# Kernel tuning notes

Hardware: AMD Instinct MI355X
Metric: run time of the kernel (lower is better)

## Reference

```python
import jax, jax.numpy as jnp
import numpy as np

NUM_USERS = 100000
NUM_ITEMS = 50000
NUM_FEATS = 512
DIM = 32
E_SOC = 3200000
E_UI = 3200000
N_PAIRS = 1000000


def setup_inputs() -> dict:
    key = jax.random.key(0)
    ks = jax.random.split(key, 14)
    return {
        "user_features": jax.random.normal(ks[0], (NUM_USERS, NUM_FEATS), jnp.float32),
        "item_features": jax.random.normal(ks[1], (NUM_ITEMS, NUM_FEATS), jnp.float32),
        "user_embedding": 0.01 * jax.random.normal(ks[2], (NUM_USERS, DIM), jnp.float32),
        "item_embedding": 0.01 * jax.random.normal(ks[3], (NUM_ITEMS, DIM), jnp.float32),
        "wr_w": jax.random.normal(ks[4], (NUM_FEATS, DIM), jnp.float32) / np.sqrt(NUM_FEATS),
        "wr_b": jax.random.normal(ks[5], (DIM,), jnp.float32) * 0.01,
        "social_rows": jax.random.randint(ks[6], (E_SOC,), 0, NUM_USERS, jnp.int32),
        "social_cols": jax.random.randint(ks[7], (E_SOC,), 0, NUM_USERS, jnp.int32),
        "social_vals": jax.random.uniform(ks[8], (E_SOC,), jnp.float32),
        "ui_rows": jax.random.randint(ks[9], (E_UI,), 0, NUM_USERS, jnp.int32),
        "ui_cols": jax.random.randint(ks[10], (E_UI,), 0, NUM_ITEMS, jnp.int32),
        "ui_vals": jax.random.uniform(ks[11], (E_UI,), jnp.float32),
        "user_indices": jax.random.randint(ks[12], (N_PAIRS,), 0, NUM_USERS, jnp.int32),
        "item_indices": jax.random.randint(ks[13], (N_PAIRS,), 0, NUM_ITEMS, jnp.int32),
    }


def _normalize(x):
    # torch .mean()/.std() over ALL elements, std unbiased (ddof=1)
    return (x - x.mean()) / jnp.std(x, ddof=1)


def _spmm(rows, cols, vals, x, n_out):
    # COO sparse @ dense: out[r] += v * x[c]
    return jax.ops.segment_sum(vals[:, None] * x[cols], rows, num_segments=n_out)


def reference(user_features, item_features, user_embedding, item_embedding,
              wr_w, wr_b, social_rows, social_cols, social_vals,
              ui_rows, ui_cols, ui_vals, user_indices, item_indices):
    n_users = user_embedding.shape[0]
    # feature normalization (done in __init__ in the torch module)
    uf = _normalize(user_features)
    itf = _normalize(item_features)

    user_reduce = _normalize(jax.nn.sigmoid(uf @ wr_w + wr_b))
    user_fusion = user_reduce + user_embedding
    item_reduce = _normalize(jax.nn.sigmoid(itf @ wr_w + wr_b))
    item_fusion = item_embedding + item_reduce

    item_consumed = _spmm(ui_rows, ui_cols, ui_vals, item_fusion, n_users)
    h1 = _spmm(social_rows, social_cols, social_vals, user_fusion, n_users)
    h2 = _spmm(social_rows, social_cols, social_vals, h1, n_users)
    last_user_embedding = item_consumed + h2

    predict_vector = jnp.sum(last_user_embedding[user_indices] * item_fusion[item_indices], axis=1)
    predictions = jax.nn.sigmoid(predict_vector)
    return predict_vector, predictions
```

## Files before the change

### kernel.cpp

```cpp
#include <hip/hip_runtime.h>
#include <hip/hip_bf16.h>

#define NU 100000
#define NI 50000
#define NF 512
#define DIM 32
#define ES 3200000
#define EU 3200000
#define NP 1000000
#define CHUNK 1024
#define NCH 98

#define ABK 32
#define BRNG 3125
#define EHALF 1600000
#define ACAP 52000
#define ATILE 2048

typedef short bf16x8 __attribute__((ext_vector_type(8)));
typedef float f32x4 __attribute__((ext_vector_type(4)));

__device__ __forceinline__ float s2f(short s) {
    unsigned u = ((unsigned)(unsigned short)s) << 16;
    return __uint_as_float(u);
}
__device__ __forceinline__ short f2bf(float f) {
    unsigned u = __float_as_uint(f);
    return (short)((u + 0x7FFFu + ((u >> 16) & 1u)) >> 16);
}

__global__ void wsum_kernel(const float* __restrict__ W, float* __restrict__ wsum) {
    int c = threadIdx.x;
    if (c >= DIM) return;
    float s = 0.f;
    for (int k = 0; k < NF; ++k) s += W[k * DIM + c];
    wsum[c] = s;
}

__global__ __launch_bounds__(256) void gemm_stats_kernel(
    const float* __restrict__ X, const float* __restrict__ W,
    float* __restrict__ RAW, float* __restrict__ statSum, float* __restrict__ statSq,
    int M)
{
    __shared__ short bfrag[16384];
    for (int idx = threadIdx.x; idx < 16384; idx += 256) {
        int j = idx & 7;
        int lane = (idx >> 3) & 63;
        int t = (idx >> 9) & 1;
        int s = idx >> 10;
        int k = s * 32 + ((lane >> 4) << 3) + j;
        int n = t * 16 + (lane & 15);
        bfrag[idx] = f2bf(W[k * DIM + n]);
    }
    __syncthreads();

    const int wave = threadIdx.x >> 6;
    const int lane = threadIdx.x & 63;
    const int quad = lane >> 4;
    const int mrow = lane & 15;

    bf16x8 ones;
#pragma unroll
    for (int j = 0; j < 8; ++j) ones[j] = (short)0x3F80;

    float lsum = 0.f, lsq = 0.f;
    const int nstrips = M >> 4;
    for (int strip = blockIdx.x * 4 + wave; strip < nstrips; strip += gridDim.x * 4) {
        const float* arow = X + (size_t)(strip * 16 + mrow) * NF + quad * 8;
        f32x4 acc0 = {0.f, 0.f, 0.f, 0.f};
        f32x4 acc1 = {0.f, 0.f, 0.f, 0.f};
        f32x4 accR = {0.f, 0.f, 0.f, 0.f};
        f32x4 accG = {0.f, 0.f, 0.f, 0.f};
#pragma unroll
        for (int s = 0; s < 16; ++s) {
            float4 a0 = *(const float4*)(arow + s * 32);
            float4 a1 = *(const float4*)(arow + s * 32 + 4);
            bf16x8 a;
            a[0] = f2bf(a0.x); a[1] = f2bf(a0.y); a[2] = f2bf(a0.z); a[3] = f2bf(a0.w);
            a[4] = f2bf(a1.x); a[5] = f2bf(a1.y); a[6] = f2bf(a1.z); a[7] = f2bf(a1.w);
            bf16x8 b0 = *(const bf16x8*)(bfrag + (s * 2 + 0) * 512 + lane * 8);
            bf16x8 b1 = *(const bf16x8*)(bfrag + (s * 2 + 1) * 512 + lane * 8);
            acc0 = __builtin_amdgcn_mfma_f32_16x16x32_bf16(a, b0, acc0, 0, 0, 0);
            acc1 = __builtin_amdgcn_mfma_f32_16x16x32_bf16(a, b1, acc1, 0, 0, 0);
            accR = __builtin_amdgcn_mfma_f32_16x16x32_bf16(a, ones, accR, 0, 0, 0);
            accG = __builtin_amdgcn_mfma_f32_16x16x32_bf16(a, a, accG, 0, 0, 0);
        }
        float* outp = RAW + (size_t)strip * 16 * DIM;
#pragma unroll
        for (int i = 0; i < 4; ++i) {
            int r = quad * 4 + i;
            outp[r * DIM + mrow]      = acc0[i];
            outp[r * DIM + 16 + mrow] = acc1[i];
        }
        if (mrow == 0) lsum += (accR[0] + accR[1]) + (accR[2] + accR[3]);
        int dg = mrow - quad * 4;
        if (dg >= 0 && dg < 4) lsq += accG[dg];
    }
#pragma unroll
    for (int off = 32; off > 0; off >>= 1) {
        lsum += __shfl_down(lsum, off);
        lsq  += __shfl_down(lsq, off);
    }
    if (lane == 0) { atomicAdd(statSum, lsum); atomicAdd(statSq, lsq); }
}

__global__ __launch_bounds__(256) void signorm_kernel(
    float* __restrict__ buf, int n4, float nx,
    const float* __restrict__ statsIn, const float* __restrict__ wsum,
    const float* __restrict__ bias, float* __restrict__ statsOut)
{
    float mu  = statsIn[0] / nx;
    float var = (statsIn[1] - nx * mu * mu) / (nx - 1.f);
    float inv = 1.f / sqrtf(var);
    float ls = 0.f, lsq = 0.f;
    int stride = gridDim.x * blockDim.x;
    for (int i = blockIdx.x * blockDim.x + threadIdx.x; i < n4; i += stride) {
        float4 v = ((const float4*)buf)[i];
        int c0 = (i << 2) & 31;
        float4 r;
        r.x = 1.f / (1.f + expf(-((v.x - mu * wsum[c0 + 0]) * inv + bias[c0 + 0])));
        r.y = 1.f / (1.f + expf(-((v.y - mu * wsum[c0 + 1]) * inv + bias[c0 + 1])));
        r.z = 1.f / (1.f + expf(-((v.z - mu * wsum[c0 + 2]) * inv + bias[c0 + 2])));
        r.w = 1.f / (1.f + expf(-((v.w - mu * wsum[c0 + 3]) * inv + bias[c0 + 3])));
        ((float4*)buf)[i] = r;
        ls  += (r.x + r.y) + (r.z + r.w);
        lsq += (r.x * r.x + r.y * r.y) + (r.z * r.z + r.w * r.w);
    }
#pragma unroll
    for (int off = 32; off > 0; off >>= 1) {
        ls  += __shfl_down(ls, off);
        lsq += __shfl_down(lsq, off);
    }
    if ((threadIdx.x & 63) == 0) { atomicAdd(statsOut + 0, ls); atomicAdd(statsOut + 1, lsq); }
}

__global__ __launch_bounds__(256) void fusion_kernel(
    float* __restrict__ buf, const float* __restrict__ emb, int n4, float n,
    const float* __restrict__ statsIn)
{
    float mu  = statsIn[0] / n;
    float var = (statsIn[1] - n * mu * mu) / (n - 1.f);
    float inv = 1.f / sqrtf(var);
    int stride = gridDim.x * blockDim.x;
    for (int i = blockIdx.x * blockDim.x + threadIdx.x; i < n4; i += stride) {
        float4 v = ((const float4*)buf)[i];
        float4 e = ((const float4*)emb)[i];
        v.x = (v.x - mu) * inv + e.x;
        v.y = (v.y - mu) * inv + e.y;
        v.z = (v.z - mu) * inv + e.z;
        v.w = (v.w - mu) * inv + e.w;
        ((float4*)buf)[i] = v;
    }
}

__global__ void hist_kernel(const int* __restrict__ sr, const int* __restrict__ ur,
                            int* __restrict__ cntS, int* __restrict__ cntU)
{
    int i = blockIdx.x * 256 + threadIdx.x;
    if (i < ES) atomicAdd(cntS + sr[i], 1);
    else        atomicAdd(cntU + ur[i - ES], 1);
}

__global__ void chunksum_kernel(const int* __restrict__ cntS, const int* __restrict__ cntU,
                                int* __restrict__ csS, int* __restrict__ csU)
{
    int b = blockIdx.x;
    const int* cnt; int* cs; int c;
    if (b < NCH) { cnt = cntS; cs = csS; c = b; }
    else         { cnt = cntU; cs = csU; c = b - NCH; }
    int base = c * CHUNK;
    int v = 0;
    for (int t = threadIdx.x; t < CHUNK; t += 256) {
        int i = base + t;
        if (i < NU) v += cnt[i];
    }
#pragma unroll
    for (int off = 32; off > 0; off >>= 1) v += __shfl_down(v, off);
    __shared__ int sm[4];
    if ((threadIdx.x & 63) == 0) sm[threadIdx.x >> 6] = v;
    __syncthreads();
    if (threadIdx.x == 0) cs[c] = sm[0] + sm[1] + sm[2] + sm[3];
}

__global__ void scan_offsets_kernel(int* __restrict__ csS, int* __restrict__ csU,
                                    int* __restrict__ rpS, int* __restrict__ rpU)
{
    if (threadIdx.x == 0) {
        int run = 0;
        for (int c = 0; c < NCH; ++c) { int t = csS[c]; csS[c] = run; run += t; }
        rpS[NU] = run;
    }
    if (threadIdx.x == 1) {
        int run = 0;
        for (int c = 0; c < NCH; ++c) { int t = csU[c]; csU[c] = run; run += t; }
        rpU[NU] = run;
    }
}

__global__ __launch_bounds__(1024) void chunkscan_kernel(
    const int* __restrict__ cntS, const int* __restrict__ cntU,
    const int* __restrict__ csS, const int* __restrict__ csU,
    int* __restrict__ rpS, int* __restrict__ rpU)
{
    int b = blockIdx.x;
    const int* cnt; const int* cs; int* rp; int c;
    if (b < NCH) { cnt = cntS; cs = csS; rp = rpS; c = b; }
    else         { cnt = cntU; cs = csU; rp = rpU; c = b - NCH; }
    int i = c * CHUNK + threadIdx.x;
    int v = (i < NU) ? cnt[i] : 0;
    __shared__ int sm[CHUNK];
    sm[threadIdx.x] = v;
    __syncthreads();
    for (int off = 1; off < CHUNK; off <<= 1) {
        int t = (threadIdx.x >= off) ? sm[threadIdx.x - off] : 0;
        __syncthreads();
        sm[threadIdx.x] += t;
        __syncthreads();
    }
    if (i < NU) rp[i] = cs[c] + sm[threadIdx.x] - v;
}

__global__ __launch_bounds__(256) void bucketA_kernel(
    const int* __restrict__ rows, const int* __restrict__ cols, const float* __restrict__ vals,
    int estart, int eend,
    unsigned* __restrict__ gW, unsigned short* __restrict__ gR, int* __restrict__ gFill)
{
    __shared__ int cnt[ABK], base[ABK], gpos[ABK], rank[ABK];
    __shared__ unsigned bufW[ATILE];
    __shared__ unsigned short bufR[ATILE];
    __shared__ unsigned char bufB[ATILE];

    int e0 = estart + blockIdx.x * ATILE;
    int n = eend - e0; if (n > ATILE) n = ATILE;
    int tid = threadIdx.x;
    if (tid < ABK) { cnt[tid] = 0; rank[tid] = 0; }
    __syncthreads();

    unsigned w[8]; unsigned short rl[8]; unsigned char bb[8]; bool ok[8];
#pragma unroll
    for (int j = 0; j < 8; ++j) {
        int idx = tid + j * 256;
        ok[j] = idx < n;
        if (ok[j]) {
            int e = e0 + idx;
            unsigned r = (unsigned)rows[e];
            unsigned b = r / BRNG;
            bb[j] = (unsigned char)b;
            rl[j] = (unsigned short)(r - b * BRNG);
            w[j]  = (((unsigned)(unsigned short)f2bf(vals[e])) << 17) | (unsigned)cols[e];
            atomicAdd(&cnt[b], 1);
        }
    }
    __syncthreads();
    if (tid == 0) {
        int run = 0;
        for (int k = 0; k < ABK; ++k) { base[k] = run; run += cnt[k]; }
    }
    __syncthreads();
    if (tid < ABK) gpos[tid] = atomicAdd(gFill + tid, cnt[tid]);
#pragma unroll
    for (int j = 0; j < 8; ++j) {
        if (ok[j]) {
            int b = bb[j];
            int p = base[b] + atomicAdd(&rank[b], 1);
            bufW[p] = w[j]; bufR[p] = rl[j]; bufB[p] = (unsigned char)b;
        }
    }
    __syncthreads();
    for (int i = tid; i < n; i += 256) {
        int b = bufB[i];
        int dst = gpos[b] + (i - base[b]);
        if (dst < ACAP) {
            gW[b * ACAP + dst] = bufW[i];
            gR[b * ACAP + dst] = bufR[i];
        }
    }
}

__global__ __launch_bounds__(256) void bucketB_kernel(
    const unsigned* __restrict__ gW, const unsigned short* __restrict__ gR,
    const int* __restrict__ gFill, const int* __restrict__ rp,
    int* __restrict__ fill, unsigned* __restrict__ csr)
{
    int myx = blockIdx.x & 7;
    int gslot = blockIdx.x >> 3;
#pragma unroll
    for (int j = 0; j < 4; ++j) {
        int b = myx + 8 * j;
        int n = gFill[b]; if (n > ACAP) n = ACAP;
        int s0 = (int)((long long)n * gslot / 128);
        int s1 = (int)((long long)n * (gslot + 1) / 128);
        for (int i = s0 + threadIdx.x; i < s1; i += 256) {
            unsigned w = gW[b * ACAP + i];
            int r = b * BRNG + (int)gR[b * ACAP + i];
            int p = rp[r] + atomicAdd(fill + r, 1);
            csr[p] = w;
        }
    }
}

__global__ __launch_bounds__(256) void spmm_csr_kernel(
    const int* __restrict__ rp, const unsigned* __restrict__ csr,
    const float* __restrict__ X, float* __restrict__ out, int accum)
{
    int r = blockIdx.x * 8 + (threadIdx.x >> 5);
    int d = threadIdx.x & 31;
    int s = rp[r], e = rp[r + 1];
    float acc = accum ? out[(size_t)r * DIM + d] : 0.f;
    float acc2 = 0.f;
    int i = s;
    for (; i + 3 < e; i += 4) {
        unsigned a = csr[i];
        unsigned b = csr[i + 1];
        unsigned c = csr[i + 2];
        unsigned dd = csr[i + 3];
        acc  += s2f((short)(a >> 17))  * X[(size_t)(a & 0x1FFFF) * DIM + d];
        acc2 += s2f((short)(b >> 17))  * X[(size_t)(b & 0x1FFFF) * DIM + d];
        acc  += s2f((short)(c >> 17))  * X[(size_t)(c & 0x1FFFF) * DIM + d];
        acc2 += s2f((short)(dd >> 17)) * X[(size_t)(dd & 0x1FFFF) * DIM + d];
    }
    for (; i < e; ++i) {
        unsigned a = csr[i];
        acc += s2f((short)(a >> 17)) * X[(size_t)(a & 0x1FFFF) * DIM + d];
    }
    out[(size_t)r * DIM + d] = acc + acc2;
}

__global__ __launch_bounds__(256) void atomic_spmm_kernel(
    const int* __restrict__ rows, const int* __restrict__ cols,
    const float* __restrict__ vals, const float* __restrict__ X,
    float* __restrict__ out, int ne)
{
    int e = blockIdx.x * 8 + (threadIdx.x >> 5);
    if (e >= ne) return;
    int d = threadIdx.x & 31;
    int r = rows[e], c = cols[e];
    atomicAdd(out + (size_t)r * DIM + d, vals[e] * X[(size_t)c * DIM + d]);
}

__global__ __launch_bounds__(256) void pairs_kernel(
    const float* __restrict__ ACC, const float* __restrict__ IF,
    const int* __restrict__ ui, const int* __restrict__ ii,
    float* __restrict__ out)
{
    int p = blockIdx.x * 8 + (threadIdx.x >> 5);
    int d = threadIdx.x & 31;
    int u = ui[p], it = ii[p];
    float v = ACC[(size_t)u * DIM + d] * IF[(size_t)it * DIM + d];
    v += __shfl_xor(v, 1);
    v += __shfl_xor(v, 2);
    v += __shfl_xor(v, 4);
    v += __shfl_xor(v, 8);
    v += __shfl_xor(v, 16);
    if (d == 0) {
        out[p] = v;
        out[NP + p] = 1.f / (1.f + expf(-v));
    }
}

extern "C" void kernel_launch(void* const* d_in, const int* in_sizes, int n_in,
                              void* d_out, int out_size, void* d_ws, size_t ws_size,
                              hipStream_t stream)
{
    const float* Xu   = (const float*)d_in[0];
    const float* Xi   = (const float*)d_in[1];
    const float* uemb = (const float*)d_in[2];
    const float* iemb = (const float*)d_in[3];
    const float* W    = (const float*)d_in[4];
    const float* bias = (const float*)d_in[5];
    const int*   sr   = (const int*)d_in[6];
    const int*   sc   = (const int*)d_in[7];
    const float* sv   = (const float*)d_in[8];
    const int*   ur   = (const int*)d_in[9];
    const int*   uc   = (const int*)d_in[10];
    const float* uv   = (const float*)d_in[11];
    const int*   uidx = (const int*)d_in[12];
    const int*   iidx = (const int*)d_in[13];
    float* out = (float*)d_out;
    (void)in_sizes; (void)n_in; (void)out_size;

    char* ws = (char*)d_ws;

    size_t o = 0;
    auto alloc = [&](size_t b) { size_t r = o; o = (o + b + 255) & ~(size_t)255; return r; };
    size_t oStats = alloc(64 * 4);
    size_t oWsum  = alloc(32 * 4);
    size_t oCntS  = alloc((size_t)NU * 4);
    size_t oCntU  = alloc((size_t)NU * 4);
    size_t oFillS = alloc((size_t)NU * 4);
    size_t oFillU = alloc((size_t)NU * 4);
    size_t oBFill = alloc(4 * ABK * 4);
    size_t oCsS   = alloc(128 * 4);
    size_t oCsU   = alloc(128 * 4);
    size_t oRpS   = alloc((size_t)(NU + 1) * 4);
    size_t oRpU   = alloc((size_t)(NU + 1) * 4);
    size_t oACC   = alloc((size_t)NU * DIM * 4);
    size_t oUF    = alloc((size_t)NU * DIM * 4);
    size_t oIF    = alloc((size_t)NI * DIM * 4);
    size_t oCsrS  = alloc((size_t)ES * 4);
    size_t oCsrU  = alloc((size_t)EU * 4);
    size_t csr_total = o;

    if (ws_size >= csr_total) {
        float*    stats = (float*)(ws + oStats);
        float*    wsum  = (float*)(ws + oWsum);
        int*      cntS  = (int*)(ws + oCntS);
        int*      cntU  = (int*)(ws + oCntU);
        int*      fillS = (int*)(ws + oFillS);
        int*      fillU = (int*)(ws + oFillU);
        int*      bf    = (int*)(ws + oBFill);
        int*      csS   = (int*)(ws + oCsS);
        int*      csU   = (int*)(ws + oCsU);
        int*      rpS   = (int*)(ws + oRpS);
        int*      rpU   = (int*)(ws + oRpU);
        float*    ACC   = (float*)(ws + oACC);
        float*    UF    = (float*)(ws + oUF);
        float*    IF    = (float*)(ws + oIF);
        unsigned* csrS  = (unsigned*)(ws + oCsrS);
        unsigned* csrU  = (unsigned*)(ws + oCsrU);
        float*    H1    = (float*)(ws + oCsrU);
        unsigned*       gW = (unsigned*)(ws + oACC);
        unsigned short* gR = (unsigned short*)(ws + oACC + (size_t)ABK * ACAP * 4);

        hipMemsetAsync(ws, 0, oCsS, stream);

        wsum_kernel<<<1, 64, 0, stream>>>(W, wsum);
        gemm_stats_kernel<<<1563, 256, 0, stream>>>(Xu, W, UF, stats + 0, stats + 1, NU);
        gemm_stats_kernel<<<782, 256, 0, stream>>>(Xi, W, IF, stats + 2, stats + 3, NI);
        signorm_kernel<<<1024, 256, 0, stream>>>(UF, NU * DIM / 4, (float)((size_t)NU * NF),
                                                 stats + 0, wsum, bias, stats + 4);
        signorm_kernel<<<512, 256, 0, stream>>>(IF, NI * DIM / 4, (float)((size_t)NI * NF),
                                                stats + 2, wsum, bias, stats + 6);
        fusion_kernel<<<1024, 256, 0, stream>>>(UF, uemb, NU * DIM / 4, (float)(NU * DIM), stats + 4);
        fusion_kernel<<<512, 256, 0, stream>>>(IF, iemb, NI * DIM / 4, (float)(NI * DIM), stats + 6);

        hist_kernel<<<(ES + EU) / 256, 256, 0, stream>>>(sr, ur, cntS, cntU);
        chunksum_kernel<<<2 * NCH, 256, 0, stream>>>(cntS, cntU, csS, csU);
        scan_offsets_kernel<<<1, 64, 0, stream>>>(csS, csU, rpS, rpU);
        chunkscan_kernel<<<2 * NCH, 1024, 0, stream>>>(cntS, cntU, csS, csU, rpS, rpU);

        const int AGRID = (EHALF + ATILE - 1) / ATILE;
        bucketA_kernel<<<AGRID, 256, 0, stream>>>(ur, uc, uv, 0, EHALF, gW, gR, bf + 0);
        bucketB_kernel<<<1024, 256, 0, stream>>>(gW, gR, bf + 0, rpU, fillU, csrU);
        bucketA_kernel<<<AGRID, 256, 0, stream>>>(ur, uc, uv, EHALF, EU, gW, gR, bf + ABK);
        bucketB_kernel<<<1024, 256, 0, stream>>>(gW, gR, bf + ABK, rpU, fillU, csrU);
        bucketA_kernel<<<AGRID, 256, 0, stream>>>(sr, sc, sv, 0, EHALF, gW, gR, bf + 2 * ABK);
        bucketB_kernel<<<1024, 256, 0, stream>>>(gW, gR, bf + 2 * ABK, rpS, fillS, csrS);
        bucketA_kernel<<<AGRID, 256, 0, stream>>>(sr, sc, sv, EHALF, ES, gW, gR, bf + 3 * ABK);
        bucketB_kernel<<<1024, 256, 0, stream>>>(gW, gR, bf + 3 * ABK, rpS, fillS, csrS);

        spmm_csr_kernel<<<NU / 8, 256, 0, stream>>>(rpU, csrU, IF, ACC, 0);
        spmm_csr_kernel<<<NU / 8, 256, 0, stream>>>(rpS, csrS, UF, H1, 0);
        spmm_csr_kernel<<<NU / 8, 256, 0, stream>>>(rpS, csrS, H1, ACC, 1);

        pairs_kernel<<<NP / 8, 256, 0, stream>>>(ACC, IF, uidx, iidx, out);
    } else {
        size_t o2 = 0;
        auto alloc2 = [&](size_t b) { size_t r = o2; o2 = (o2 + b + 255) & ~(size_t)255; return r; };
        size_t aStats = alloc2(64 * 4);
        size_t aWsum  = alloc2(32 * 4);
        size_t aACC   = alloc2((size_t)NU * DIM * 4);
        size_t aH1    = alloc2((size_t)NU * DIM * 4);
        size_t aUF    = alloc2((size_t)NU * DIM * 4);
        size_t aIF    = alloc2((size_t)NI * DIM * 4);

        float* stats = (float*)(ws + aStats);
        float* wsum  = (float*)(ws + aWsum);
        float* ACC   = (float*)(ws + aACC);
        float* H1    = (float*)(ws + aH1);
        float* UF    = (float*)(ws + aUF);
        float* IF    = (float*)(ws + aIF);

        hipMemsetAsync(ws, 0, 512, stream);
        hipMemsetAsync(ws + aACC, 0, (size_t)NU * DIM * 8, stream);

        wsum_kernel<<<1, 64, 0, stream>>>(W, wsum);
        gemm_stats_kernel<<<1563, 256, 0, stream>>>(Xu, W, UF, stats + 0, stats + 1, NU);
        gemm_stats_kernel<<<782, 256, 0, stream>>>(Xi, W, IF, stats + 2, stats + 3, NI);
        signorm_kernel<<<1024, 256, 0, stream>>>(UF, NU * DIM / 4, (float)((size_t)NU * NF),
                                                 stats + 0, wsum, bias, stats + 4);
        signorm_kernel<<<512, 256, 0, stream>>>(IF, NI * DIM / 4, (float)((size_t)NI * NF),
                                                stats + 2, wsum, bias, stats + 6);
        fusion_kernel<<<1024, 256, 0, stream>>>(UF, uemb, NU * DIM / 4, (float)(NU * DIM), stats + 4);
        fusion_kernel<<<512, 256, 0, stream>>>(IF, iemb, NI * DIM / 4, (float)(NI * DIM), stats + 6);

        atomic_spmm_kernel<<<EU / 8, 256, 0, stream>>>(ur, uc, uv, IF, ACC, EU);
        atomic_spmm_kernel<<<ES / 8, 256, 0, stream>>>(sr, sc, sv, UF, H1, ES);
        atomic_spmm_kernel<<<ES / 8, 256, 0, stream>>>(sr, sc, sv, H1, ACC, ES);

        pairs_kernel<<<NP / 8, 256, 0, stream>>>(ACC, IF, uidx, iidx, out);
    }
}
```

Measured before the change: 1.702 ms.

## Build per-half CSR from bucketed rows with LDS histograms instead of global atomics

Replaces the global-atomic row histogram over all 6.4M edges with a per-half histogram computed from the already bucketed row indices, using a shared-memory histogram per bucket slice. Each edge half now gets its own row-pointer array and CSR segment, and the SpMM kernel walks two segments per row. This removes heavily contended global atomics on the original row arrays. In exchange it launches many more small scan kernels (four rounds of chunksum, scan and chunkscan) and adds a second segment loop per row in the SpMM.

```diff
diff --git a/kernel.cpp b/kernel.cpp
--- a/kernel.cpp
+++ b/kernel.cpp
@@ -16,6 +16,7 @@
 #define EHALF 1600000
 #define ACAP 52000
 #define ATILE 2048
+#define HSUB 8
 
 typedef short bf16x8 __attribute__((ext_vector_type(8)));
 typedef float f32x4 __attribute__((ext_vector_type(4)));
@@ -153,73 +154,6 @@
     }
 }
 
-__global__ void hist_kernel(const int* __restrict__ sr, const int* __restrict__ ur,
-                            int* __restrict__ cntS, int* __restrict__ cntU)
-{
-    int i = blockIdx.x * 256 + threadIdx.x;
-    if (i < ES) atomicAdd(cntS + sr[i], 1);
-    else        atomicAdd(cntU + ur[i - ES], 1);
-}
-
-__global__ void chunksum_kernel(const int* __restrict__ cntS, const int* __restrict__ cntU,
-                                int* __restrict__ csS, int* __restrict__ csU)
-{
-    int b = blockIdx.x;
-    const int* cnt; int* cs; int c;
-    if (b < NCH) { cnt = cntS; cs = csS; c = b; }
-    else         { cnt = cntU; cs = csU; c = b - NCH; }
-    int base = c * CHUNK;
-    int v = 0;
-    for (int t = threadIdx.x; t < CHUNK; t += 256) {
-        int i = base + t;
-        if (i < NU) v += cnt[i];
-    }
-#pragma unroll
-    for (int off = 32; off > 0; off >>= 1) v += __shfl_down(v, off);
-    __shared__ int sm[4];
-    if ((threadIdx.x & 63) == 0) sm[threadIdx.x >> 6] = v;
-    __syncthreads();
-    if (threadIdx.x == 0) cs[c] = sm[0] + sm[1] + sm[2] + sm[3];
-}
-
-__global__ void scan_offsets_kernel(int* __restrict__ csS, int* __restrict__ csU,
-                                    int* __restrict__ rpS, int* __restrict__ rpU)
-{
-    if (threadIdx.x == 0) {
-        int run = 0;
-        for (int c = 0; c < NCH; ++c) { int t = csS[c]; csS[c] = run; run += t; }
-        rpS[NU] = run;
-    }
-    if (threadIdx.x == 1) {
-        int run = 0;
-        for (int c = 0; c < NCH; ++c) { int t = csU[c]; csU[c] = run; run += t; }
-        rpU[NU] = run;
-    }
-}
-
-__global__ __launch_bounds__(1024) void chunkscan_kernel(
-    const int* __restrict__ cntS, const int* __restrict__ cntU,
-    const int* __restrict__ csS, const int* __restrict__ csU,
-    int* __restrict__ rpS, int* __restrict__ rpU)
-{
-    int b = blockIdx.x;
-    const int* cnt; const int* cs; int* rp; int c;
-    if (b < NCH) { cnt = cntS; cs = csS; rp = rpS; c = b; }
-    else         { cnt = cntU; cs = csU; rp = rpU; c = b - NCH; }
-    int i = c * CHUNK + threadIdx.x;
-    int v = (i < NU) ? cnt[i] : 0;
-    __shared__ int sm[CHUNK];
-    sm[threadIdx.x] = v;
-    __syncthreads();
-    for (int off = 1; off < CHUNK; off <<= 1) {
-        int t = (threadIdx.x >= off) ? sm[threadIdx.x - off] : 0;
-        __syncthreads();
-        sm[threadIdx.x] += t;
-        __syncthreads();
-    }
-    if (i < NU) rp[i] = cs[c] + sm[threadIdx.x] - v;
-}
-
 __global__ __launch_bounds__(256) void bucketA_kernel(
     const int* __restrict__ rows, const int* __restrict__ cols, const float* __restrict__ vals,
     int estart, int eend,
@@ -277,6 +211,78 @@
     }
 }
 
+__global__ __launch_bounds__(256) void bucket_hist_kernel(
+    const unsigned short* __restrict__ gR, const int* __restrict__ gFill,
+    int* __restrict__ cnt)
+{
+    __shared__ int h[BRNG];
+    int x = blockIdx.x;
+    int b = (x & 7) + 8 * ((x >> 6) & 3);
+    int sub = (x >> 3) & 7;
+    for (int i = threadIdx.x; i < BRNG; i += 256) h[i] = 0;
+    __syncthreads();
+    int n = gFill[b]; if (n > ACAP) n = ACAP;
+    int s0 = (int)((long long)n * sub / HSUB);
+    int s1 = (int)((long long)n * (sub + 1) / HSUB);
+    for (int i = s0 + threadIdx.x; i < s1; i += 256)
+        atomicAdd(&h[gR[b * ACAP + i]], 1);
+    __syncthreads();
+    int base = b * BRNG;
+    for (int i = threadIdx.x; i < BRNG; i += 256) {
+        int v = h[i];
+        if (v) atomicAdd(cnt + base + i, v);
+    }
+}
+
+__global__ void chunksum_kernel(const int* __restrict__ cnt, int* __restrict__ cs)
+{
+    int c = blockIdx.x;
+    int base = c * CHUNK;
+    int v = 0;
+    for (int t = threadIdx.x; t < CHUNK; t += 256) {
+        int i = base + t;
+        if (i < NU) v += cnt[i];
+    }
+#pragma unroll
+    for (int off = 32; off > 0; off >>= 1) v += __shfl_down(v, off);
+    __shared__ int sm[4];
+    if ((threadIdx.x & 63) == 0) sm[threadIdx.x >> 6] = v;
+    __syncthreads();
+    if (threadIdx.x == 0) cs[c] = sm[0] + sm[1] + sm[2] + sm[3];
+}
+
+__global__ void scan_offsets_kernel(int* __restrict__ cs, int* __restrict__ rp)
+{
+    if (threadIdx.x == 0) {
+        int run = 0;
+        for (int c = 0; c < NCH; ++c) { int t = cs[c]; cs[c] = run; run += t; }
+        rp[NU] = run;
+    }
+}
+
+__global__ __launch_bounds__(1024) void chunkscan_kernel(
+    int* __restrict__ cnt, const int* __restrict__ cs,
+    int* __restrict__ rp, int* __restrict__ fill)
+{
+    int c = blockIdx.x;
+    int i = c * CHUNK + threadIdx.x;
+    int v = (i < NU) ? cnt[i] : 0;
+    __shared__ int sm[CHUNK];
+    sm[threadIdx.x] = v;
+    __syncthreads();
+    for (int off = 1; off < CHUNK; off <<= 1) {
+        int t = (threadIdx.x >= off) ? sm[threadIdx.x - off] : 0;
+        __syncthreads();
+        sm[threadIdx.x] += t;
+        __syncthreads();
+    }
+    if (i < NU) {
+        rp[i] = cs[c] + sm[threadIdx.x] - v;
+        cnt[i] = 0;
+        fill[i] = 0;
+    }
+}
+
 __global__ __launch_bounds__(256) void bucketB_kernel(
     const unsigned* __restrict__ gW, const unsigned short* __restrict__ gR,
     const int* __restrict__ gFill, const int* __restrict__ rp,
@@ -299,15 +305,10 @@
     }
 }
 
-__global__ __launch_bounds__(256) void spmm_csr_kernel(
-    const int* __restrict__ rp, const unsigned* __restrict__ csr,
-    const float* __restrict__ X, float* __restrict__ out, int accum)
-{
-    int r = blockIdx.x * 8 + (threadIdx.x >> 5);
-    int d = threadIdx.x & 31;
-    int s = rp[r], e = rp[r + 1];
-    float acc = accum ? out[(size_t)r * DIM + d] : 0.f;
-    float acc2 = 0.f;
+__device__ __forceinline__ void spmm_seg(
+    const unsigned* __restrict__ csr, int s, int e,
+    const float* __restrict__ X, int d, float& acc, float& acc2)
+{
     int i = s;
     for (; i + 3 < e; i += 4) {
         unsigned a = csr[i];
@@ -323,6 +324,19 @@
         unsigned a = csr[i];
         acc += s2f((short)(a >> 17)) * X[(size_t)(a & 0x1FFFF) * DIM + d];
     }
+}
+
+__global__ __launch_bounds__(256) void spmm_csr_kernel(
+    const int* __restrict__ rp0, const int* __restrict__ rp1,
+    const unsigned* __restrict__ csr,
+    const float* __restrict__ X, float* __restrict__ out, int accum)
+{
+    int r = blockIdx.x * 8 + (threadIdx.x >> 5);
+    int d = threadIdx.x & 31;
+    float acc = accum ? out[(size_t)r * DIM + d] : 0.f;
+    float acc2 = 0.f;
+    spmm_seg(csr, rp0[r], rp0[r + 1], X, d, acc, acc2);
+    spmm_seg(csr, EHALF + rp1[r], EHALF + rp1[r + 1], X, d, acc, acc2);
     out[(size_t)r * DIM + d] = acc + acc2;
 }
 
@@ -385,15 +399,14 @@
     auto alloc = [&](size_t b) { size_t r = o; o = (o + b + 255) & ~(size_t)255; return r; };
     size_t oStats = alloc(64 * 4);
     size_t oWsum  = alloc(32 * 4);
-    size_t oCntS  = alloc((size_t)NU * 4);
-    size_t oCntU  = alloc((size_t)NU * 4);
-    size_t oFillS = alloc((size_t)NU * 4);
-    size_t oFillU = alloc((size_t)NU * 4);
+    size_t oCnt   = alloc((size_t)NU * 4);
+    size_t oFill  = alloc((size_t)NU * 4);
     size_t oBFill = alloc(4 * ABK * 4);
-    size_t oCsS   = alloc(128 * 4);
-    size_t oCsU   = alloc(128 * 4);
-    size_t oRpS   = alloc((size_t)(NU + 1) * 4);
-    size_t oRpU   = alloc((size_t)(NU + 1) * 4);
+    size_t oCs    = alloc(128 * 4);
+    size_t oRpU0  = alloc((size_t)(NU + 1) * 4);
+    size_t oRpU1  = alloc((size_t)(NU + 1) * 4);
+    size_t oRpS0  = alloc((size_t)(NU + 1) * 4);
+    size_t oRpS1  = alloc((size_t)(NU + 1) * 4);
     size_t oACC   = alloc((size_t)NU * DIM * 4);
     size_t oUF    = alloc((size_t)NU * DIM * 4);
     size_t oIF    = alloc((size_t)NI * DIM * 4);
@@ -404,15 +417,14 @@
     if (ws_size >= csr_total) {
         float*    stats = (float*)(ws + oStats);
         float*    wsum  = (float*)(ws + oWsum);
-        int*      cntS  = (int*)(ws + oCntS);
-        int*      cntU  = (int*)(ws + oCntU);
-        int*      fillS = (int*)(ws + oFillS);
-        int*      fillU = (int*)(ws + oFillU);
+        int*      cnt   = (int*)(ws + oCnt);
+        int*      fill  = (int*)(ws + oFill);
         int*      bf    = (int*)(ws + oBFill);
-        int*      csS   = (int*)(ws + oCsS);
-        int*      csU   = (int*)(ws + oCsU);
-        int*      rpS   = (int*)(ws + oRpS);
-        int*      rpU   = (int*)(ws + oRpU);
+        int*      cs    = (int*)(ws + oCs);
+        int*      rpU0  = (int*)(ws + oRpU0);
+        int*      rpU1  = (int*)(ws + oRpU1);
+        int*      rpS0  = (int*)(ws + oRpS0);
+        int*      rpS1  = (int*)(ws + oRpS1);
         float*    ACC   = (float*)(ws + oACC);
         float*    UF    = (float*)(ws + oUF);
         float*    IF    = (float*)(ws + oIF);
@@ -422,7 +434,7 @@
         unsigned*       gW = (unsigned*)(ws + oACC);
         unsigned short* gR = (unsigned short*)(ws + oACC + (size_t)ABK * ACAP * 4);
 
-        hipMemsetAsync(ws, 0, oCsS, stream);
+        hipMemsetAsync(ws, 0, oCs, stream);
 
         wsum_kernel<<<1, 64, 0, stream>>>(W, wsum);
         gemm_stats_kernel<<<1563, 256, 0, stream>>>(Xu, W, UF, stats + 0, stats + 1, NU);
@@ -434,24 +446,37 @@
         fusion_kernel<<<1024, 256, 0, stream>>>(UF, uemb, NU * DIM / 4, (float)(NU * DIM), stats + 4);
         fusion_kernel<<<512, 256, 0, stream>>>(IF, iemb, NI * DIM / 4, (float)(NI * DIM), stats + 6);
 
-        hist_kernel<<<(ES + EU) / 256, 256, 0, stream>>>(sr, ur, cntS, cntU);
-        chunksum_kernel<<<2 * NCH, 256, 0, stream>>>(cntS, cntU, csS, csU);
-        scan_offsets_kernel<<<1, 64, 0, stream>>>(csS, csU, rpS, rpU);
-        chunkscan_kernel<<<2 * NCH, 1024, 0, stream>>>(cntS, cntU, csS, csU, rpS, rpU);
-
         const int AGRID = (EHALF + ATILE - 1) / ATILE;
+        const int HGRID = ABK * HSUB;
+
         bucketA_kernel<<<AGRID, 256, 0, stream>>>(ur, uc, uv, 0, EHALF, gW, gR, bf + 0);
-        bucketB_kernel<<<1024, 256, 0, stream>>>(gW, gR, bf + 0, rpU, fillU, csrU);
+        bucket_hist_kernel<<<HGRID, 256, 0, stream>>>(gR, bf + 0, cnt);
+        chunksum_kernel<<<NCH, 256, 0, stream>>>(cnt, cs);
+        scan_offsets_kernel<<<1, 64, 0, stream>>>(cs, rpU0);
+        chunkscan_kernel<<<NCH, 1024, 0, stream>>>(cnt, cs, rpU0, fill);
+        bucketB_kernel<<<1024, 256, 0, stream>>>(gW, gR, bf + 0, rpU0, fill, csrU);
         bucketA_kernel<<<AGRID, 256, 0, stream>>>(ur, uc, uv, EHALF, EU, gW, gR, bf + ABK);
-        bucketB_kernel<<<1024, 256, 0, stream>>>(gW, gR, bf + ABK, rpU, fillU, csrU);
+        bucket_hist_kernel<<<HGRID, 256, 0, stream>>>(gR, bf + ABK, cnt);
+        chunksum_kernel<<<NCH, 256, 0, stream>>>(cnt, cs);
+        scan_offsets_kernel<<<1, 64, 0, stream>>>(cs, rpU1);
+        chunkscan_kernel<<<NCH, 1024, 0, stream>>>(cnt, cs, rpU1, fill);
+        bucketB_kernel<<<1024, 256, 0, stream>>>(gW, gR, bf + ABK, rpU1, fill, csrU + EHALF);
         bucketA_kernel<<<AGRID, 256, 0, stream>>>(sr, sc, sv, 0, EHALF, gW, gR, bf + 2 * ABK);
-        bucketB_kernel<<<1024, 256, 0, stream>>>(gW, gR, bf + 2 * ABK, rpS, fillS, csrS);
+        bucket_hist_kernel<<<HGRID, 256, 0, stream>>>(gR, bf + 2 * ABK, cnt);
+        chunksum_kernel<<<NCH, 256, 0, stream>>>(cnt, cs);
+        scan_offsets_kernel<<<1, 64, 0, stream>>>(cs, rpS0);
+        chunkscan_kernel<<<NCH, 1024, 0, stream>>>(cnt, cs, rpS0, fill);
+        bucketB_kernel<<<1024, 256, 0, stream>>>(gW, gR, bf + 2 * ABK, rpS0, fill, csrS);
         bucketA_kernel<<<AGRID, 256, 0, stream>>>(sr, sc, sv, EHALF, ES, gW, gR, bf + 3 * ABK);
-        bucketB_kernel<<<1024, 256, 0, stream>>>(gW, gR, bf + 3 * ABK, rpS, fillS, csrS);
-
-        spmm_csr_kernel<<<NU / 8, 256, 0, stream>>>(rpU, csrU, IF, ACC, 0);
-        spmm_csr_kernel<<<NU / 8, 256, 0, stream>>>(rpS, csrS, UF, H1, 0);
-        spmm_csr_kernel<<<NU / 8, 256, 0, stream>>>(rpS, csrS, H1, ACC, 1);
+        bucket_hist_kernel<<<HGRID, 256, 0, stream>>>(gR, bf + 3 * ABK, cnt);
+        chunksum_kernel<<<NCH, 256, 0, stream>>>(cnt, cs);
+        scan_offsets_kernel<<<1, 64, 0, stream>>>(cs, rpS1);
+        chunkscan_kernel<<<NCH, 1024, 0, stream>>>(cnt, cs, rpS1, fill);
+        bucketB_kernel<<<1024, 256, 0, stream>>>(gW, gR, bf + 3 * ABK, rpS1, fill, csrS + EHALF);
+
+        spmm_csr_kernel<<<NU / 8, 256, 0, stream>>>(rpU0, rpU1, csrU, IF, ACC, 0);
+        spmm_csr_kernel<<<NU / 8, 256, 0, stream>>>(rpS0, rpS1, csrS, UF, H1, 0);
+        spmm_csr_kernel<<<NU / 8, 256, 0, stream>>>(rpS0, rpS1, csrS, H1, ACC, 1);
 
         pairs_kernel<<<NP / 8, 256, 0, stream>>>(ACC, IF, uidx, iidx, out);
     } else {
```

After: 1.541 ms. -9.5%, faster.
